# Performance work log

Hardware: AMD Instinct MI355X
Metric: run time of the kernel (lower is better)

Reference implementation:

```python
import jax, jax.numpy as jnp
import numpy as np

N_NODES = 1_000_000
EMB_DIM = 128
BATCH = 65536
N_NEG = 20
EPS = 1e-9


def setup_inputs() -> dict:
    key = jax.random.key(0)
    k1, k2, k3, k4, k5 = jax.random.split(key, 5)
    # Xavier-uniform bound for an (N, D) embedding matrix
    bound = float(np.sqrt(6.0 / (N_NODES + EMB_DIM)))
    center_w = jax.random.uniform(k1, (N_NODES, EMB_DIM), jnp.float32, -bound, bound)
    context_w = jax.random.uniform(k2, (N_NODES, EMB_DIM), jnp.float32, -bound, bound)
    center_nodes = jax.random.randint(k3, (BATCH,), 0, N_NODES, dtype=jnp.int64 if jax.config.jax_enable_x64 else jnp.int32)
    context_nodes = jax.random.randint(k4, (BATCH,), 0, N_NODES, dtype=center_nodes.dtype)
    negative_nodes = jax.random.randint(k5, (BATCH, N_NEG), 0, N_NODES, dtype=center_nodes.dtype)
    return {
        "center_nodes": center_nodes,
        "context_nodes": context_nodes,
        "negative_nodes": negative_nodes,
        "center_w": center_w,
        "context_w": context_w,
    }


def reference(center_nodes, context_nodes, negative_nodes, center_w, context_w):
    center_emb = center_w[center_nodes]          # [B, D]
    context_emb = context_w[context_nodes]       # [B, D]
    negative_emb = context_w[negative_nodes]     # [B, K, D]

    pos_score = jnp.sum(center_emb * context_emb, axis=1)          # [B]
    pos_loss = -jnp.log(jax.nn.sigmoid(pos_score) + EPS)           # [B]

    neg_score = jnp.einsum("bkd,bd->bk", negative_emb, center_emb)  # [B, K]
    neg_loss = -jnp.sum(jnp.log(jax.nn.sigmoid(-neg_score) + EPS), axis=1)  # [B]

    return jnp.mean(pos_loss + neg_loss)
```

## Files before the change

### kernel.cpp

```cpp
#include <hip/hip_runtime.h>


constexpr int NNEG = 20;
constexpr int D = 128;
constexpr int NBLOCKS = 2048;

__global__ __launch_bounds__(256) void n2v_loss_kernel(
    const int* __restrict__ center_nodes,
    const int* __restrict__ context_nodes,
    const int* __restrict__ negative_nodes,
    const float* __restrict__ center_w,
    const float* __restrict__ context_w,
    float* __restrict__ block_partials,
    int batch)
{
    const int lane    = threadIdx.x & 63;
    const int half    = lane >> 5;
    const int sublane = lane & 31;
    const int wave    = threadIdx.x >> 6;
    const int wpb     = blockDim.x >> 6;
    const int gwave   = blockIdx.x * wpb + wave;
    const int nwav    = gridDim.x * wpb;

    float acc = 0.0f;

    for (int b0 = gwave * 2; b0 < batch; b0 += nwav * 2) {
        const int b = b0 + half;
        float loss = 0.0f;

        if (b < batch) {
            const int ci = center_nodes[b];
            const int xi = context_nodes[b];

            const float4* crow = reinterpret_cast<const float4*>(center_w  + (size_t)ci * D);
            const float4* xrow = reinterpret_cast<const float4*>(context_w + (size_t)xi * D);
            const float4  ce = crow[sublane];
            const float4  xe = xrow[sublane];

            int nb[NNEG];
            {
                const int4* np4 = reinterpret_cast<const int4*>(negative_nodes + (size_t)b * NNEG);
#pragma unroll
                for (int q = 0; q < 5; ++q) {
                    const int4 v = np4[q];
                    nb[q * 4 + 0] = v.x; nb[q * 4 + 1] = v.y;
                    nb[q * 4 + 2] = v.z; nb[q * 4 + 3] = v.w;
                }
            }

            float sc[NNEG + 1];
            sc[0] = fmaf(ce.x, xe.x, fmaf(ce.y, xe.y, fmaf(ce.z, xe.z, ce.w * xe.w)));

#pragma unroll
            for (int k = 0; k < NNEG; ++k) {
                const float4* nrow =
                    reinterpret_cast<const float4*>(context_w + (size_t)nb[k] * D);
                const float4 ne = nrow[sublane];
                sc[k + 1] = fmaf(ce.x, ne.x, fmaf(ce.y, ne.y, fmaf(ce.z, ne.z, ce.w * ne.w)));
            }

#pragma unroll
            for (int k = 0; k <= NNEG; ++k) {
                float v = sc[k];
#pragma unroll
                for (int off = 16; off > 0; off >>= 1)
                    v += __shfl_xor(v, off, 64);
                sc[k] = v;
            }

            float p0 = 1.0f + __expf(-sc[0]);
            float p1 = 1.0f;
#pragma unroll
            for (int k = 1; k <= NNEG - 1; k += 2)
                p0 *= (1.0f + __expf(sc[k]));
#pragma unroll
            for (int k = 2; k <= NNEG; k += 2)
                p1 *= (1.0f + __expf(sc[k]));
            loss = __logf(p0 * p1);
        }

        acc += loss;
    }

    acc += __shfl_xor(acc, 32, 64);

    __shared__ float wsum[8];
    if (lane == 0) wsum[wave] = acc;
    __syncthreads();
    if (threadIdx.x == 0) {
        float s = 0.0f;
        for (int w = 0; w < wpb; ++w) s += wsum[w];
        block_partials[blockIdx.x] = s;
    }
}

__global__ __launch_bounds__(256) void n2v_reduce_kernel(
    const float* __restrict__ partials, int n, float inv_batch,
    float* __restrict__ out)
{
    __shared__ float sm[256];
    float v = 0.0f;
    for (int i = threadIdx.x; i < n; i += 256) v += partials[i];
    sm[threadIdx.x] = v;
    __syncthreads();
    for (int s = 128; s > 0; s >>= 1) {
        if (threadIdx.x < s) sm[threadIdx.x] += sm[threadIdx.x + s];
        __syncthreads();
    }
    if (threadIdx.x == 0) out[0] = sm[0] * inv_batch;
}

extern "C" void kernel_launch(void* const* d_in, const int* in_sizes, int n_in,
                              void* d_out, int out_size, void* d_ws, size_t ws_size,
                              hipStream_t stream) {
    const int*   center_nodes   = (const int*)d_in[0];
    const int*   context_nodes  = (const int*)d_in[1];
    const int*   negative_nodes = (const int*)d_in[2];
    const float* center_w       = (const float*)d_in[3];
    const float* context_w      = (const float*)d_in[4];
    float*       out            = (float*)d_out;
    const int    batch          = in_sizes[0];

    float* partials = (float*)d_ws;

    n2v_loss_kernel<<<NBLOCKS, 256, 0, stream>>>(
        center_nodes, context_nodes, negative_nodes,
        center_w, context_w, partials, batch);

    n2v_reduce_kernel<<<1, 256, 0, stream>>>(
        partials, NBLOCKS, 1.0f / (float)batch, out);
}
```

Before: 115.2 us.

## Assign eight batch rows per wave with 8-lane groups per row

Each wavefront now handles eight batch rows at once: every 8-lane group owns one row, and each lane loads four float4 chunks per embedding row instead of one. This cuts the cross-lane shuffle reduction from five steps to three per score and puts more independent row gathers in flight per wave. In exchange it raises per-thread register use (four float4 center chunks plus 21 scores), which may lower occupancy. The loss accumulator now needs extra shuffles at the end to fold the eight groups together.

```diff
diff --git a/kernel.cpp b/kernel.cpp
--- a/kernel.cpp
+++ b/kernel.cpp
@@ -14,18 +14,18 @@
     float* __restrict__ block_partials,
     int batch)
 {
-    const int lane    = threadIdx.x & 63;
-    const int half    = lane >> 5;
-    const int sublane = lane & 31;
-    const int wave    = threadIdx.x >> 6;
-    const int wpb     = blockDim.x >> 6;
-    const int gwave   = blockIdx.x * wpb + wave;
-    const int nwav    = gridDim.x * wpb;
+    const int lane  = threadIdx.x & 63;
+    const int grp   = lane >> 3;
+    const int gl    = lane & 7;
+    const int wave  = threadIdx.x >> 6;
+    const int wpb   = blockDim.x >> 6;
+    const int gwave = blockIdx.x * wpb + wave;
+    const int nwav  = gridDim.x * wpb;
 
     float acc = 0.0f;
 
-    for (int b0 = gwave * 2; b0 < batch; b0 += nwav * 2) {
-        const int b = b0 + half;
+    for (int b0 = gwave * 8; b0 < batch; b0 += nwav * 8) {
+        const int b = b0 + grp;
         float loss = 0.0f;
 
         if (b < batch) {
@@ -34,8 +34,10 @@
 
             const float4* crow = reinterpret_cast<const float4*>(center_w  + (size_t)ci * D);
             const float4* xrow = reinterpret_cast<const float4*>(context_w + (size_t)xi * D);
-            const float4  ce = crow[sublane];
-            const float4  xe = xrow[sublane];
+
+            float4 ce[4];
+#pragma unroll
+            for (int q = 0; q < 4; ++q) ce[q] = crow[gl + q * 8];
 
             int nb[NNEG];
             {
@@ -49,21 +51,40 @@
             }
 
             float sc[NNEG + 1];
-            sc[0] = fmaf(ce.x, xe.x, fmaf(ce.y, xe.y, fmaf(ce.z, xe.z, ce.w * xe.w)));
+            {
+                float d0 = 0.0f, d1 = 0.0f, d2 = 0.0f, d3 = 0.0f;
+#pragma unroll
+                for (int q = 0; q < 4; ++q) {
+                    const float4 xe = xrow[gl + q * 8];
+                    d0 = fmaf(ce[q].x, xe.x, d0);
+                    d1 = fmaf(ce[q].y, xe.y, d1);
+                    d2 = fmaf(ce[q].z, xe.z, d2);
+                    d3 = fmaf(ce[q].w, xe.w, d3);
+                }
+                sc[0] = (d0 + d1) + (d2 + d3);
+            }
 
 #pragma unroll
             for (int k = 0; k < NNEG; ++k) {
                 const float4* nrow =
                     reinterpret_cast<const float4*>(context_w + (size_t)nb[k] * D);
-                const float4 ne = nrow[sublane];
-                sc[k + 1] = fmaf(ce.x, ne.x, fmaf(ce.y, ne.y, fmaf(ce.z, ne.z, ce.w * ne.w)));
+                float d0 = 0.0f, d1 = 0.0f, d2 = 0.0f, d3 = 0.0f;
+#pragma unroll
+                for (int q = 0; q < 4; ++q) {
+                    const float4 ne = nrow[gl + q * 8];
+                    d0 = fmaf(ce[q].x, ne.x, d0);
+                    d1 = fmaf(ce[q].y, ne.y, d1);
+                    d2 = fmaf(ce[q].z, ne.z, d2);
+                    d3 = fmaf(ce[q].w, ne.w, d3);
+                }
+                sc[k + 1] = (d0 + d1) + (d2 + d3);
             }
 
 #pragma unroll
             for (int k = 0; k <= NNEG; ++k) {
                 float v = sc[k];
 #pragma unroll
-                for (int off = 16; off > 0; off >>= 1)
+                for (int off = 4; off > 0; off >>= 1)
                     v += __shfl_xor(v, off, 64);
                 sc[k] = v;
             }
@@ -82,6 +103,8 @@
         acc += loss;
     }
 
+    acc += __shfl_xor(acc, 8, 64);
+    acc += __shfl_xor(acc, 16, 64);
     acc += __shfl_xor(acc, 32, 64);
 
     __shared__ float wsum[8];
```

Measured after the change: 119.1 us. 3.4% more time.
